# Kernel tuning notes

Measured on AMD Instinct MI355X. Metric: run time of the kernel, lower is better.

The kernel has to match this reference:

```python
import jax, jax.numpy as jnp
import numpy as np

OVERLAP_THRESHOLD = 0.5
NEG_POS_RATIO = 3
ALPHA = 1.0


def cxcy_to_xy(cxcy):
    return jnp.concatenate([cxcy[..., :2] - cxcy[..., 2:] / 2,
                            cxcy[..., :2] + cxcy[..., 2:] / 2], axis=-1)


def xy_to_cxcy(xy):
    return jnp.concatenate([(xy[..., :2] + xy[..., 2:]) / 2,
                            xy[..., 2:] - xy[..., :2]], axis=-1)


def cxcy_to_gcxgcy(cxcy, priors_cxcy):
    return jnp.concatenate([
        (cxcy[..., :2] - priors_cxcy[..., :2]) / (priors_cxcy[..., 2:] / 10.0),
        jnp.log(cxcy[..., 2:] / priors_cxcy[..., 2:]) * 5.0], axis=-1)


def jaccard(a, b):
    # a: [N,4] xy, b: [P,4] xy -> [N,P]
    lo = jnp.maximum(a[:, None, :2], b[None, :, :2])
    hi = jnp.minimum(a[:, None, 2:], b[None, :, 2:])
    inter = jnp.prod(jnp.clip(hi - lo, 0.0), axis=-1)  # [N,P]
    area_a = jnp.prod(a[:, 2:] - a[:, :2], axis=-1)  # [N]
    area_b = jnp.prod(b[:, 2:] - b[:, :2], axis=-1)  # [P]
    return inter / (area_a[:, None] + area_b[None, :] - inter)


def _match_one(boxes_i, labels_i, priors_cxcy, priors_xy):
    n_objects = boxes_i.shape[0]
    overlap = jaccard(boxes_i, priors_xy)  # [N,P]
    overlap_for_each_prior = overlap.max(axis=0)  # [P]
    object_for_each_prior = overlap.argmax(axis=0)  # [P]
    prior_for_each_object = overlap.argmax(axis=1)  # [N]
    # force each object to own its best prior
    object_for_each_prior = object_for_each_prior.at[prior_for_each_object].set(
        jnp.arange(n_objects))
    overlap_for_each_prior = overlap_for_each_prior.at[prior_for_each_object].set(1.0)
    labels_for_each_prior = labels_i[object_for_each_prior]
    labels_for_each_prior = jnp.where(overlap_for_each_prior < OVERLAP_THRESHOLD,
                                      0, labels_for_each_prior)
    matched = boxes_i[object_for_each_prior]  # [P,4]
    true_locs = cxcy_to_gcxgcy(xy_to_cxcy(matched), priors_cxcy)  # [P,4]
    return true_locs, labels_for_each_prior


def reference(predicted_locs, predicted_scores, boxes, labels, priors_cxcy):
    B, P, C = predicted_scores.shape
    priors_xy = cxcy_to_xy(priors_cxcy)
    true_locs, true_classes = jax.vmap(
        _match_one, in_axes=(0, 0, None, None))(boxes, labels, priors_cxcy, priors_xy)
    # true_locs: [B,P,4], true_classes: [B,P]
    positive = true_classes != 0  # [B,P]
    n_pos = positive.sum(axis=1)  # [B]
    n_pos_total = n_pos.sum()

    # SmoothL1 (beta=1, mean over selected elements = n_pos_total*4)
    d = predicted_locs - true_locs
    ad = jnp.abs(d)
    sl1 = jnp.where(ad < 1.0, 0.5 * d * d, ad - 0.5)  # [B,P,4]
    loc_loss = (sl1 * positive[..., None]).sum() / (n_pos_total.astype(jnp.float32) * 4.0)

    # per-prior cross-entropy
    logp = jax.nn.log_softmax(predicted_scores, axis=-1)  # [B,P,C]
    conf_all = -jnp.take_along_axis(logp, true_classes[..., None], axis=-1)[..., 0]  # [B,P]

    conf_pos_sum = jnp.where(positive, conf_all, 0.0).sum()
    conf_neg = jnp.where(positive, 0.0, conf_all)
    conf_neg_sorted = jnp.sort(conf_neg, axis=1)[:, ::-1]  # descending
    n_hard_neg = NEG_POS_RATIO * n_pos  # [B]
    rank = jnp.arange(P)[None, :]
    hard_neg_mask = rank < n_hard_neg[:, None]
    conf_hard_neg_sum = jnp.where(hard_neg_mask, conf_neg_sorted, 0.0).sum()

    conf_loss = (conf_hard_neg_sum + conf_pos_sum) / n_pos_total.astype(jnp.float32)
    return conf_loss + ALPHA * loc_loss


def setup_inputs() -> dict:
    key = jax.random.key(0)
    ks = jax.random.split(key, 7)
    B, P, C, N = 128, 8732, 21, 16
    predicted_locs = jax.random.normal(ks[0], (B, P, 4), dtype=jnp.float32)
    predicted_scores = jax.random.normal(ks[1], (B, P, C), dtype=jnp.float32)
    # valid xy boxes in [0,1]
    p1 = jax.random.uniform(ks[2], (B, N, 2)) * 0.85
    wh = jax.random.uniform(ks[3], (B, N, 2), minval=0.02, maxval=0.15)
    boxes = jnp.concatenate([p1, jnp.minimum(p1 + wh, 1.0)], axis=-1)
    labels = jax.random.randint(ks[4], (B, N), 1, C)
    cxcy = jax.random.uniform(ks[5], (P, 2))
    pwh = jax.random.uniform(ks[6], (P, 2), minval=0.05, maxval=0.5)
    priors_cxcy = jnp.concatenate([cxcy, pwh], axis=-1)
    return {"predicted_locs": predicted_locs, "predicted_scores": predicted_scores,
            "boxes": boxes, "labels": labels, "priors_cxcy": priors_cxcy}
```

## Files before the change

kernel.cpp:

```cpp
#include <hip/hip_runtime.h>


#define MAXN 16
#define MAXE 16

__device__ __forceinline__ float sl1f(float d) {
    float ad = fabsf(d);
    return ad < 1.0f ? 0.5f * d * d : ad - 0.5f;
}

__global__ __launch_bounds__(256) void k_pre(
    const float* __restrict__ boxes,
    const float* __restrict__ priors,
    int P, int N,
    int* __restrict__ pfo,
    int* __restrict__ npos,
    float* __restrict__ acc)
{
    __shared__ float rin[4], run[4];
    __shared__ int   rid[4];
    const int id = blockIdx.x;
    const int tid = threadIdx.x;
    const int lane = tid & 63, wid = tid >> 6;

    if (tid == 0 && (id % N) == 0) npos[id / N] = 0;
    if (id == 0 && tid < 2) ((unsigned*)acc)[tid] = 0u;

    const float* bp = boxes + (size_t)id * 4;
    const float bx1 = bp[0], by1 = bp[1], bx2 = bp[2], by2 = bp[3];
    const float ba = (bx2 - bx1) * (by2 - by1);

    float bi = -1.0f, bu = 1.0f; int idx = 0x7fffffff;
#pragma unroll 2
    for (int p = tid; p < P; p += 256) {
        float4 pr = ((const float4*)priors)[p];
        float px1 = pr.x - pr.z * 0.5f, py1 = pr.y - pr.w * 0.5f;
        float px2 = pr.x + pr.z * 0.5f, py2 = pr.y + pr.w * 0.5f;
        float parea = (px2 - px1) * (py2 - py1);
        float iw = fmaxf(fminf(bx2, px2) - fmaxf(bx1, px1), 0.0f);
        float ih = fmaxf(fminf(by2, py2) - fmaxf(by1, py1), 0.0f);
        float in = iw * ih;
        float un = ba + parea - in;
        if (in * bu > bi * un) { bi = in; bu = un; idx = p; }
    }
#pragma unroll
    for (int off = 32; off > 0; off >>= 1) {
        float oin = __shfl_down(bi, off);
        float oun = __shfl_down(bu, off);
        int   oid = __shfl_down(idx, off);
        float a = oin * bu, c = bi * oun;
        if (a > c || (a == c && oid < idx)) { bi = oin; bu = oun; idx = oid; }
    }
    if (lane == 0) { rin[wid] = bi; run[wid] = bu; rid[wid] = idx; }
    __syncthreads();
    if (tid == 0) {
        for (int w = 1; w < 4; w++) {
            float oin = rin[w], oun = run[w]; int oid = rid[w];
            float a = oin * bu, c = bi * oun;
            if (a > c || (a == c && oid < idx)) { bi = oin; bu = oun; idx = oid; }
        }
        pfo[id] = idx;
    }
}

template<int CT>
__global__ __launch_bounds__(256) void k_fused(
    const float* __restrict__ plocs,
    const float* __restrict__ scores,
    const float* __restrict__ boxes,
    const int*   __restrict__ labels,
    const float* __restrict__ priors,
    const int*   __restrict__ pfo,
    int P, int Crt, int N, int nchunk,
    float* __restrict__ conf_out,
    int*   __restrict__ npos,
    float* __restrict__ locpart,
    float* __restrict__ pospart)
{
    const int C = CT > 0 ? CT : Crt;
    extern __shared__ float sh[];
    __shared__ float sx1[MAXN], sy1[MAXN], sx2[MAXN], sy2[MAXN], barea[MAXN];
    __shared__ int   blab[MAXN], spfo[MAXN];
    __shared__ float redf[4], redp[4];
    __shared__ int   redi[4];

    const int b = blockIdx.y;
    const int tid = threadIdx.x;
    const int lane = tid & 63, wid = tid >> 6;
    if (N > MAXN) N = MAXN;
    const int p0 = blockIdx.x * 256;
    const int rows = min(256, P - p0);

    if (tid < N) {
        const float* bp = boxes + ((size_t)b * N + tid) * 4;
        float x1 = bp[0], y1 = bp[1], x2 = bp[2], y2 = bp[3];
        sx1[tid] = x1; sy1[tid] = y1; sx2[tid] = x2; sy2[tid] = y2;
        barea[tid] = (x2 - x1) * (y2 - y1);
        blab[tid] = labels[(size_t)b * N + tid];
        spfo[tid] = pfo[b * N + tid];
    }

    {
        const size_t f4base = ((size_t)b * P + p0) * C / 4;
        const int f4cnt = (rows * C + 3) / 4;
        const float4* __restrict__ s4 = (const float4*)scores;
        for (int j = tid; j < f4cnt; j += 256)
            ((float4*)sh)[j] = s4[f4base + j];
    }
    __syncthreads();

    const int p = p0 + tid;
    float locs = 0.0f, posc = 0.0f, conf = 0.0f;
    int np = 0;
    if (p < P) {
        float4 pr = ((const float4*)priors)[p];
        float px1 = pr.x - pr.z * 0.5f, py1 = pr.y - pr.w * 0.5f;
        float px2 = pr.x + pr.z * 0.5f, py2 = pr.y + pr.w * 0.5f;
        float parea = (px2 - px1) * (py2 - py1);
        float bi = -1.0f, bu = 1.0f; int bestn = 0;
#pragma unroll
        for (int n = 0; n < MAXN; n++) {
            if (n < N) {
                float iw = fmaxf(fminf(sx2[n], px2) - fmaxf(sx1[n], px1), 0.0f);
                float ih = fmaxf(fminf(sy2[n], py2) - fmaxf(sy1[n], py1), 0.0f);
                float in = iw * ih;
                float un = barea[n] + parea - in;
                if (in * bu > bi * un) { bi = in; bu = un; bestn = n; }
            }
        }
#pragma unroll
        for (int n = 0; n < MAXN; n++) {
            if (n < N && spfo[n] == p) { bestn = n; bi = 1.0f; bu = 1.0f; }
        }
        const int lab = (bi < 0.5f * bu) ? 0 : blab[bestn];

        const float* r = sh + tid * C;
        float m = -3.402823466e38f;
#pragma unroll
        for (int c = 0; c < C; c++) m = fmaxf(m, r[c]);
        float sum = 0.0f;
#pragma unroll
        for (int c = 0; c < C; c++) sum += __expf(r[c] - m);
        float ce = m + __logf(sum) - r[lab];

        if (lab != 0) {
            posc = ce; np = 1;
            int n = bestn;
            float cx = (sx1[n] + sx2[n]) * 0.5f, cy = (sy1[n] + sy2[n]) * 0.5f;
            float w = sx2[n] - sx1[n], h = sy2[n] - sy1[n];
            float g0 = (cx - pr.x) / (pr.z / 10.0f);
            float g1 = (cy - pr.y) / (pr.w / 10.0f);
            float g2 = logf(w / pr.z) * 5.0f;
            float g3 = logf(h / pr.w) * 5.0f;
            float4 pl = ((const float4*)plocs)[(size_t)b * P + p];
            locs = sl1f(pl.x - g0) + sl1f(pl.y - g1) + sl1f(pl.z - g2) + sl1f(pl.w - g3);
        } else {
            conf = ce;
        }
        conf_out[(size_t)b * P + p] = conf;
    }
#pragma unroll
    for (int off = 32; off > 0; off >>= 1) {
        locs += __shfl_down(locs, off);
        posc += __shfl_down(posc, off);
        np   += __shfl_down(np, off);
    }
    if (lane == 0) { redf[wid] = locs; redp[wid] = posc; redi[wid] = np; }
    __syncthreads();
    if (tid == 0) {
        float L = redf[0] + redf[1] + redf[2] + redf[3];
        float Pp = redp[0] + redp[1] + redp[2] + redp[3];
        int   c = redi[0] + redi[1] + redi[2] + redi[3];
        if (c) atomicAdd(&npos[b], c);
        locpart[b * nchunk + blockIdx.x] = L;
        pospart[b * nchunk + blockIdx.x] = Pp;
    }
}

__global__ __launch_bounds__(1024, 4) void k_hard(
    const float* __restrict__ conf,
    const int* __restrict__ npos,
    const float* __restrict__ locpart,
    const float* __restrict__ pospart,
    int P, int B, int nloc,
    float* __restrict__ acc,
    float* __restrict__ out)
{
    __shared__ int   redi[16 * 3];
    __shared__ float redf2[16];
    __shared__ int   redi2[16];
    __shared__ float rl[16], rp[16];
    __shared__ int   rn[16], is_last;
    const int b = blockIdx.x, tid = threadIdx.x;
    const int lane = tid & 63, wid = tid >> 6;
    const int nthr = blockDim.x, nw = nthr >> 6;
    const int ne = (P + nthr - 1) / nthr;
    long long kk = (long long)npos[b] * 3;
    int k = kk > P ? P : (int)kk;

    float S = 0.0f;
    if (k > 0) {
        unsigned e[MAXE];
#pragma unroll
        for (int j = 0; j < MAXE; j++) {
            int p = j * nthr + tid;
            e[j] = (j < ne && p < P) ? __float_as_uint(conf[(size_t)b * P + p]) : 0u;
        }

        unsigned lo = 0u, hi = 0x7F800000u;
        while (lo < hi) {
            unsigned span = hi - lo;
            if (span >= 8) {
                unsigned q = span >> 2;
                unsigned m1 = lo + q, m2 = lo + 2 * q, m3 = lo + 3 * q;
                int c1 = 0, c2 = 0, c3 = 0;
#pragma unroll
                for (int j = 0; j < MAXE; j++) {
                    if (j < ne) {
                        unsigned v = e[j];
                        c1 += (int)__popcll(__ballot(v >= m1));
                        c2 += (int)__popcll(__ballot(v >= m2));
                        c3 += (int)__popcll(__ballot(v >= m3));
                    }
                }
                if (lane == 0) {
                    redi[wid * 3 + 0] = c1; redi[wid * 3 + 1] = c2; redi[wid * 3 + 2] = c3;
                }
                __syncthreads();
                int C1 = 0, C2 = 0, C3 = 0;
                for (int w = 0; w < nw; w++) {
                    C1 += redi[w * 3 + 0]; C2 += redi[w * 3 + 1]; C3 += redi[w * 3 + 2];
                }
                __syncthreads();
                if      (C3 >= k) lo = m3;
                else if (C2 >= k) { lo = m2; hi = m3 - 1; }
                else if (C1 >= k) { lo = m1; hi = m2 - 1; }
                else              hi = m1 - 1;
            } else {
                unsigned mid = lo + ((span + 1) >> 1);
                int c = 0;
#pragma unroll
                for (int j = 0; j < MAXE; j++)
                    if (j < ne) c += (int)__popcll(__ballot(e[j] >= mid));
                if (lane == 0) redi[wid * 3] = c;
                __syncthreads();
                int Cc = 0;
                for (int w = 0; w < nw; w++) Cc += redi[w * 3];
                __syncthreads();
                if (Cc >= k) lo = mid; else hi = mid - 1;
            }
        }

        float t = __uint_as_float(lo);
        float sgt = 0.0f; int cgt = 0;
#pragma unroll
        for (int j = 0; j < MAXE; j++) {
            if (j < ne) {
                float v = __uint_as_float(e[j]);
                if (v > t) { sgt += v; cgt++; }
            }
        }
#pragma unroll
        for (int off = 32; off > 0; off >>= 1) {
            sgt += __shfl_down(sgt, off);
            cgt += __shfl_down(cgt, off);
        }
        if (lane == 0) { redf2[wid] = sgt; redi2[wid] = cgt; }
        __syncthreads();
        if (tid == 0) {
            int Cg = 0;
            for (int w = 0; w < nw; w++) { S += redf2[w]; Cg += redi2[w]; }
            S += (float)(k - Cg) * t;
        }
        __syncthreads();
    }

    if (tid == 0) {
        atomicAdd(&acc[0], S);
        __threadfence();
        unsigned tk = atomicAdd((unsigned*)(acc + 1), 1u);
        is_last = (tk == (unsigned)gridDim.x - 1) ? 1 : 0;
    }
    __syncthreads();
    if (is_last) {
        float lp = 0.0f, pp = 0.0f; int np = 0;
        for (int i = tid; i < nloc; i += nthr) { lp += locpart[i]; pp += pospart[i]; }
        for (int i = tid; i < B; i += nthr) np += npos[i];
#pragma unroll
        for (int off = 32; off > 0; off >>= 1) {
            lp += __shfl_down(lp, off);
            pp += __shfl_down(pp, off);
            np += __shfl_down(np, off);
        }
        if (lane == 0) { rl[wid] = lp; rp[wid] = pp; rn[wid] = np; }
        __syncthreads();
        if (tid == 0) {
            float L = 0.0f, Pp = 0.0f; int Np = 0;
            for (int w = 0; w < nw; w++) { L += rl[w]; Pp += rp[w]; Np += rn[w]; }
            float hard = atomicAdd(&acc[0], 0.0f);
            float npf = (float)Np;
            out[0] = (hard + Pp) / npf + L / (npf * 4.0f);
        }
    }
}

extern "C" void kernel_launch(void* const* d_in, const int* in_sizes, int n_in,
                              void* d_out, int out_size, void* d_ws, size_t ws_size,
                              hipStream_t stream)
{
    const float* plocs  = (const float*)d_in[0];
    const float* scores = (const float*)d_in[1];
    const float* boxes  = (const float*)d_in[2];
    const int*   labels = (const int*)d_in[3];
    const float* priors = (const float*)d_in[4];

    int P = in_sizes[4] / 4;
    int B = in_sizes[0] / (P * 4);
    int C = in_sizes[1] / (in_sizes[0] / 4);
    int N = in_sizes[3] / B;
    int nchunk = (P + 255) / 256;
    int nloc = B * nchunk;
    int BN = B * N;

    char* w = (char*)d_ws;
    float* slot    = (float*)w;  w += (size_t)B * P * sizeof(float);
    int*   npos    = (int*)w;    w += (size_t)B * sizeof(int);
    int*   pfo     = (int*)w;    w += (size_t)BN * sizeof(int);
    float* locpart = (float*)w;  w += (size_t)nloc * sizeof(float);
    float* pospart = (float*)w;  w += (size_t)nloc * sizeof(float);
    w = (char*)(((uintptr_t)w + 63) & ~(uintptr_t)63);
    float* acc     = (float*)w;

    k_pre<<<BN, 256, 0, stream>>>(boxes, priors, P, N, pfo, npos, acc);

    dim3 ga(nchunk, B);
    size_t smf = (size_t)256 * C * sizeof(float);
    if (C == 21) {
        k_fused<21><<<ga, 256, smf, stream>>>(plocs, scores, boxes, labels, priors,
                                              pfo, P, C, N, nchunk, slot, npos,
                                              locpart, pospart);
    } else {
        k_fused<0><<<ga, 256, smf, stream>>>(plocs, scores, boxes, labels, priors,
                                             pfo, P, C, N, nchunk, slot, npos,
                                             locpart, pospart);
    }

    k_hard<<<B, 1024, 0, stream>>>(slot, npos, locpart, pospart,
                                   P, B, nloc, acc, (float*)d_out);
}
```

Measured before the change: 213.8 us.

## Remove prior-matching pre-kernel and apply forced-match corrections inside hard-negative kernel

Drops the separate k_pre launch that found each object's best prior. The fused kernel now computes unforced matches and writes per-chunk positive counts instead of doing atomics. The hard-negative kernel recomputes each object's best prior per image and applies delta corrections to the loc, positive-CE and positive-count sums, then zeroes those priors' conf entries before selection. This saves one launch and its serial dependency, at the cost of extra per-block prior scanning in k_hard with 16 register accumulators per thread.

Measured after the change: 692.2 us. 224% more time.

```diff
diff --git a/kernel.cpp b/kernel.cpp
--- a/kernel.cpp
+++ b/kernel.cpp
@@ -7,60 +7,6 @@
 __device__ __forceinline__ float sl1f(float d) {
     float ad = fabsf(d);
     return ad < 1.0f ? 0.5f * d * d : ad - 0.5f;
-}
-
-__global__ __launch_bounds__(256) void k_pre(
-    const float* __restrict__ boxes,
-    const float* __restrict__ priors,
-    int P, int N,
-    int* __restrict__ pfo,
-    int* __restrict__ npos,
-    float* __restrict__ acc)
-{
-    __shared__ float rin[4], run[4];
-    __shared__ int   rid[4];
-    const int id = blockIdx.x;
-    const int tid = threadIdx.x;
-    const int lane = tid & 63, wid = tid >> 6;
-
-    if (tid == 0 && (id % N) == 0) npos[id / N] = 0;
-    if (id == 0 && tid < 2) ((unsigned*)acc)[tid] = 0u;
-
-    const float* bp = boxes + (size_t)id * 4;
-    const float bx1 = bp[0], by1 = bp[1], bx2 = bp[2], by2 = bp[3];
-    const float ba = (bx2 - bx1) * (by2 - by1);
-
-    float bi = -1.0f, bu = 1.0f; int idx = 0x7fffffff;
-#pragma unroll 2
-    for (int p = tid; p < P; p += 256) {
-        float4 pr = ((const float4*)priors)[p];
-        float px1 = pr.x - pr.z * 0.5f, py1 = pr.y - pr.w * 0.5f;
-        float px2 = pr.x + pr.z * 0.5f, py2 = pr.y + pr.w * 0.5f;
-        float parea = (px2 - px1) * (py2 - py1);
-        float iw = fmaxf(fminf(bx2, px2) - fmaxf(bx1, px1), 0.0f);
-        float ih = fmaxf(fminf(by2, py2) - fmaxf(by1, py1), 0.0f);
-        float in = iw * ih;
-        float un = ba + parea - in;
-        if (in * bu > bi * un) { bi = in; bu = un; idx = p; }
-    }
-#pragma unroll
-    for (int off = 32; off > 0; off >>= 1) {
-        float oin = __shfl_down(bi, off);
-        float oun = __shfl_down(bu, off);
-        int   oid = __shfl_down(idx, off);
-        float a = oin * bu, c = bi * oun;
-        if (a > c || (a == c && oid < idx)) { bi = oin; bu = oun; idx = oid; }
-    }
-    if (lane == 0) { rin[wid] = bi; run[wid] = bu; rid[wid] = idx; }
-    __syncthreads();
-    if (tid == 0) {
-        for (int w = 1; w < 4; w++) {
-            float oin = rin[w], oun = run[w]; int oid = rid[w];
-            float a = oin * bu, c = bi * oun;
-            if (a > c || (a == c && oid < idx)) { bi = oin; bu = oun; idx = oid; }
-        }
-        pfo[id] = idx;
-    }
 }
 
 template<int CT>
@@ -70,34 +16,35 @@
     const float* __restrict__ boxes,
     const int*   __restrict__ labels,
     const float* __restrict__ priors,
-    const int*   __restrict__ pfo,
     int P, int Crt, int N, int nchunk,
     float* __restrict__ conf_out,
-    int*   __restrict__ npos,
     float* __restrict__ locpart,
-    float* __restrict__ pospart)
+    float* __restrict__ pospart,
+    int*   __restrict__ nppart,
+    unsigned* __restrict__ acc)
 {
     const int C = CT > 0 ? CT : Crt;
     extern __shared__ float sh[];
-    __shared__ float sx1[MAXN], sy1[MAXN], sx2[MAXN], sy2[MAXN], barea[MAXN];
-    __shared__ int   blab[MAXN], spfo[MAXN];
+    __shared__ float sx1[MAXN], sy1[MAXN], sx2[MAXN], sy2[MAXN], sba[MAXN];
+    __shared__ int   blab[MAXN];
     __shared__ float redf[4], redp[4];
     __shared__ int   redi[4];
 
     const int b = blockIdx.y;
     const int tid = threadIdx.x;
     const int lane = tid & 63, wid = tid >> 6;
-    if (N > MAXN) N = MAXN;
+    int Nc = N > MAXN ? MAXN : N;
     const int p0 = blockIdx.x * 256;
     const int rows = min(256, P - p0);
 
-    if (tid < N) {
+    if (blockIdx.x == 0 && b == 0 && tid < 2) acc[tid] = 0u;
+
+    if (tid < Nc) {
         const float* bp = boxes + ((size_t)b * N + tid) * 4;
         float x1 = bp[0], y1 = bp[1], x2 = bp[2], y2 = bp[3];
         sx1[tid] = x1; sy1[tid] = y1; sx2[tid] = x2; sy2[tid] = y2;
-        barea[tid] = (x2 - x1) * (y2 - y1);
+        sba[tid] = (x2 - x1) * (y2 - y1);
         blab[tid] = labels[(size_t)b * N + tid];
-        spfo[tid] = pfo[b * N + tid];
     }
 
     {
@@ -120,28 +67,36 @@
         float bi = -1.0f, bu = 1.0f; int bestn = 0;
 #pragma unroll
         for (int n = 0; n < MAXN; n++) {
-            if (n < N) {
+            if (n < Nc) {
                 float iw = fmaxf(fminf(sx2[n], px2) - fmaxf(sx1[n], px1), 0.0f);
                 float ih = fmaxf(fminf(sy2[n], py2) - fmaxf(sy1[n], py1), 0.0f);
                 float in = iw * ih;
-                float un = barea[n] + parea - in;
+                float un = sba[n] + parea - in;
                 if (in * bu > bi * un) { bi = in; bu = un; bestn = n; }
             }
         }
-#pragma unroll
-        for (int n = 0; n < MAXN; n++) {
-            if (n < N && spfo[n] == p) { bestn = n; bi = 1.0f; bu = 1.0f; }
-        }
         const int lab = (bi < 0.5f * bu) ? 0 : blab[bestn];
 
         const float* r = sh + tid * C;
-        float m = -3.402823466e38f;
-#pragma unroll
-        for (int c = 0; c < C; c++) m = fmaxf(m, r[c]);
-        float sum = 0.0f;
-#pragma unroll
-        for (int c = 0; c < C; c++) sum += __expf(r[c] - m);
-        float ce = m + __logf(sum) - r[lab];
+        float ce;
+        if constexpr (CT > 0) {
+            float rv[CT];
+#pragma unroll
+            for (int c = 0; c < CT; c++) rv[c] = r[c];
+            float m = -3.402823466e38f;
+#pragma unroll
+            for (int c = 0; c < CT; c++) m = fmaxf(m, rv[c]);
+            float sum = 0.0f;
+#pragma unroll
+            for (int c = 0; c < CT; c++) sum += __expf(rv[c] - m);
+            ce = m + __logf(sum) - r[lab];
+        } else {
+            float m = -3.402823466e38f;
+            for (int c = 0; c < C; c++) m = fmaxf(m, r[c]);
+            float sum = 0.0f;
+            for (int c = 0; c < C; c++) sum += __expf(r[c] - m);
+            ce = m + __logf(sum) - r[lab];
+        }
 
         if (lab != 0) {
             posc = ce; np = 1;
@@ -168,37 +123,184 @@
     if (lane == 0) { redf[wid] = locs; redp[wid] = posc; redi[wid] = np; }
     __syncthreads();
     if (tid == 0) {
-        float L = redf[0] + redf[1] + redf[2] + redf[3];
-        float Pp = redp[0] + redp[1] + redp[2] + redp[3];
-        int   c = redi[0] + redi[1] + redi[2] + redi[3];
-        if (c) atomicAdd(&npos[b], c);
-        locpart[b * nchunk + blockIdx.x] = L;
-        pospart[b * nchunk + blockIdx.x] = Pp;
+        locpart[b * nchunk + blockIdx.x] = redf[0] + redf[1] + redf[2] + redf[3];
+        pospart[b * nchunk + blockIdx.x] = redp[0] + redp[1] + redp[2] + redp[3];
+        nppart [b * nchunk + blockIdx.x] = redi[0] + redi[1] + redi[2] + redi[3];
     }
 }
 
 __global__ __launch_bounds__(1024, 4) void k_hard(
+    const float* __restrict__ plocs,
+    const float* __restrict__ scores,
+    const float* __restrict__ boxes,
+    const int*   __restrict__ labels,
+    const float* __restrict__ priors,
     const float* __restrict__ conf,
-    const int* __restrict__ npos,
     const float* __restrict__ locpart,
     const float* __restrict__ pospart,
-    int P, int B, int nloc,
-    float* __restrict__ acc,
+    const int*   __restrict__ nppart,
+    int P, int C, int N, int nchunk, int B, int nloc,
+    float* __restrict__ hardpart,
+    float* __restrict__ locfix,
+    float* __restrict__ posfix,
+    int*   __restrict__ nposc,
+    unsigned* __restrict__ acc,
     float* __restrict__ out)
 {
-    __shared__ int   redi[16 * 3];
-    __shared__ float redf2[16];
-    __shared__ int   redi2[16];
-    __shared__ float rl[16], rp[16];
-    __shared__ int   rn[16], is_last;
+    __shared__ float sx1[MAXN], sy1[MAXN], sx2[MAXN], sy2[MAXN], sba[MAXN];
+    __shared__ int   blab[MAXN];
+    __shared__ float win[16 * MAXN], wun[16 * MAXN];
+    __shared__ int   widx[16 * MAXN];
+    __shared__ int   fixp[MAXN];
+    __shared__ float rfa[16], rfb[16];
+    __shared__ int   ria[16], rib[16];
+    __shared__ int   srch[16 * 3];
+    __shared__ int   s_np, is_last;
+    __shared__ float s_dloc, s_dpos;
+
     const int b = blockIdx.x, tid = threadIdx.x;
     const int lane = tid & 63, wid = tid >> 6;
     const int nthr = blockDim.x, nw = nthr >> 6;
+    int Nc = N > MAXN ? MAXN : N;
+
+    if (tid < Nc) {
+        const float* bp = boxes + ((size_t)b * N + tid) * 4;
+        float x1 = bp[0], y1 = bp[1], x2 = bp[2], y2 = bp[3];
+        sx1[tid] = x1; sy1[tid] = y1; sx2[tid] = x2; sy2[tid] = y2;
+        sba[tid] = (x2 - x1) * (y2 - y1);
+        blab[tid] = labels[(size_t)b * N + tid];
+    }
+    __syncthreads();
+
+    {
+        float bin[MAXN], bun[MAXN]; int bix[MAXN];
+#pragma unroll
+        for (int n = 0; n < MAXN; n++) { bin[n] = -1.0f; bun[n] = 1.0f; bix[n] = 0x7fffffff; }
+        for (int p = tid; p < P; p += nthr) {
+            float4 pr = ((const float4*)priors)[p];
+            float px1 = pr.x - pr.z * 0.5f, py1 = pr.y - pr.w * 0.5f;
+            float px2 = pr.x + pr.z * 0.5f, py2 = pr.y + pr.w * 0.5f;
+            float parea = (px2 - px1) * (py2 - py1);
+#pragma unroll
+            for (int n = 0; n < MAXN; n++) {
+                if (n < Nc) {
+                    float iw = fmaxf(fminf(sx2[n], px2) - fmaxf(sx1[n], px1), 0.0f);
+                    float ih = fmaxf(fminf(sy2[n], py2) - fmaxf(sy1[n], py1), 0.0f);
+                    float in = iw * ih;
+                    float un = sba[n] + parea - in;
+                    if (in * bun[n] > bin[n] * un) { bin[n] = in; bun[n] = un; bix[n] = p; }
+                }
+            }
+        }
+#pragma unroll
+        for (int n = 0; n < MAXN; n++) {
+            if (n < Nc) {
+                float i_ = bin[n], u_ = bun[n]; int x_ = bix[n];
+#pragma unroll
+                for (int off = 32; off > 0; off >>= 1) {
+                    float oi = __shfl_down(i_, off);
+                    float ou = __shfl_down(u_, off);
+                    int   ox = __shfl_down(x_, off);
+                    float a = oi * u_, c = i_ * ou;
+                    if (a > c || (a == c && ox < x_)) { i_ = oi; u_ = ou; x_ = ox; }
+                }
+                if (lane == 0) { win[wid * MAXN + n] = i_; wun[wid * MAXN + n] = u_; widx[wid * MAXN + n] = x_; }
+            }
+        }
+        __syncthreads();
+        if (tid < Nc) {
+            float i_ = win[tid], u_ = wun[tid]; int x_ = widx[tid];
+            for (int w = 1; w < nw; w++) {
+                float oi = win[w * MAXN + tid], ou = wun[w * MAXN + tid];
+                int   ox = widx[w * MAXN + tid];
+                float a = oi * u_, c = i_ * ou;
+                if (a > c || (a == c && ox < x_)) { i_ = oi; u_ = ou; x_ = ox; }
+            }
+            fixp[tid] = x_;
+        }
+        __syncthreads();
+    }
+
+    float dloc = 0.0f, dpos = 0.0f; int dnp = 0;
+    if (tid < Nc) {
+        int pn = fixp[tid];
+        bool active = true;
+        for (int n2 = tid + 1; n2 < Nc; n2++) if (fixp[n2] == pn) active = false;
+        if (active) {
+            float4 pr = ((const float4*)priors)[pn];
+            float px1 = pr.x - pr.z * 0.5f, py1 = pr.y - pr.w * 0.5f;
+            float px2 = pr.x + pr.z * 0.5f, py2 = pr.y + pr.w * 0.5f;
+            float parea = (px2 - px1) * (py2 - py1);
+            float bi = -1.0f, bu = 1.0f; int bestn = 0;
+#pragma unroll
+            for (int n = 0; n < MAXN; n++) {
+                if (n < Nc) {
+                    float iw = fmaxf(fminf(sx2[n], px2) - fmaxf(sx1[n], px1), 0.0f);
+                    float ih = fmaxf(fminf(sy2[n], py2) - fmaxf(sy1[n], py1), 0.0f);
+                    float in = iw * ih;
+                    float un = sba[n] + parea - in;
+                    if (in * bu > bi * un) { bi = in; bu = un; bestn = n; }
+                }
+            }
+            const int lab0 = (bi < 0.5f * bu) ? 0 : blab[bestn];
+
+            const float* r = scores + ((size_t)b * P + pn) * C;
+            float m = -3.402823466e38f;
+            for (int c = 0; c < C; c++) m = fmaxf(m, r[c]);
+            float sum = 0.0f;
+            for (int c = 0; c < C; c++) sum += __expf(r[c] - m);
+            const float lse = m + __logf(sum);
+
+            float4 pl = ((const float4*)plocs)[(size_t)b * P + pn];
+            {
+                int n = tid;
+                float cx = (sx1[n] + sx2[n]) * 0.5f, cy = (sy1[n] + sy2[n]) * 0.5f;
+                float w = sx2[n] - sx1[n], h = sy2[n] - sy1[n];
+                float g0 = (cx - pr.x) / (pr.z / 10.0f);
+                float g1 = (cy - pr.y) / (pr.w / 10.0f);
+                float g2 = logf(w / pr.z) * 5.0f;
+                float g3 = logf(h / pr.w) * 5.0f;
+                dloc = sl1f(pl.x - g0) + sl1f(pl.y - g1) + sl1f(pl.z - g2) + sl1f(pl.w - g3);
+                dpos = lse - r[blab[n]];
+            }
+            if (lab0 != 0) {
+                int n = bestn;
+                float cx = (sx1[n] + sx2[n]) * 0.5f, cy = (sy1[n] + sy2[n]) * 0.5f;
+                float w = sx2[n] - sx1[n], h = sy2[n] - sy1[n];
+                float g0 = (cx - pr.x) / (pr.z / 10.0f);
+                float g1 = (cy - pr.y) / (pr.w / 10.0f);
+                float g2 = logf(w / pr.z) * 5.0f;
+                float g3 = logf(h / pr.w) * 5.0f;
+                dloc -= sl1f(pl.x - g0) + sl1f(pl.y - g1) + sl1f(pl.z - g2) + sl1f(pl.w - g3);
+                dpos -= lse - r[lab0];
+            } else {
+                dnp = 1;
+            }
+        }
+    }
+    int npp = 0;
+    for (int i = tid; i < nchunk; i += nthr) npp += nppart[b * nchunk + i];
+#pragma unroll
+    for (int off = 32; off > 0; off >>= 1) {
+        dloc += __shfl_down(dloc, off);
+        dpos += __shfl_down(dpos, off);
+        dnp  += __shfl_down(dnp, off);
+        npp  += __shfl_down(npp, off);
+    }
+    if (lane == 0) { rfa[wid] = dloc; rfb[wid] = dpos; ria[wid] = dnp; rib[wid] = npp; }
+    __syncthreads();
+    if (tid == 0) {
+        float L = 0.0f, Pp = 0.0f; int a = 0, c = 0;
+        for (int w = 0; w < nw; w++) { L += rfa[w]; Pp += rfb[w]; a += ria[w]; c += rib[w]; }
+        s_dloc = L; s_dpos = Pp; s_np = c + a;
+    }
+    __syncthreads();
+    const int npos_b = s_np;
+    long long kk = (long long)npos_b * 3;
+    int k = kk > P ? P : (int)kk;
+
+    float S = 0.0f;
     const int ne = (P + nthr - 1) / nthr;
-    long long kk = (long long)npos[b] * 3;
-    int k = kk > P ? P : (int)kk;
-
-    float S = 0.0f;
     if (k > 0) {
         unsigned e[MAXE];
 #pragma unroll
@@ -206,7 +308,13 @@
             int p = j * nthr + tid;
             e[j] = (j < ne && p < P) ? __float_as_uint(conf[(size_t)b * P + p]) : 0u;
         }
-
+#pragma unroll
+        for (int j = 0; j < MAXE; j++) {
+            if (j < ne) {
+                int p = j * nthr + tid;
+                for (int n = 0; n < Nc; n++) if (fixp[n] == p) e[j] = 0u;
+            }
+        }
         unsigned lo = 0u, hi = 0x7F800000u;
         while (lo < hi) {
             unsigned span = hi - lo;
@@ -223,13 +331,11 @@
                         c3 += (int)__popcll(__ballot(v >= m3));
                     }
                 }
-                if (lane == 0) {
-                    redi[wid * 3 + 0] = c1; redi[wid * 3 + 1] = c2; redi[wid * 3 + 2] = c3;
-                }
+                if (lane == 0) { srch[wid * 3] = c1; srch[wid * 3 + 1] = c2; srch[wid * 3 + 2] = c3; }
                 __syncthreads();
                 int C1 = 0, C2 = 0, C3 = 0;
                 for (int w = 0; w < nw; w++) {
-                    C1 += redi[w * 3 + 0]; C2 += redi[w * 3 + 1]; C3 += redi[w * 3 + 2];
+                    C1 += srch[w * 3]; C2 += srch[w * 3 + 1]; C3 += srch[w * 3 + 2];
                 }
                 __syncthreads();
                 if      (C3 >= k) lo = m3;
@@ -242,15 +348,14 @@
 #pragma unroll
                 for (int j = 0; j < MAXE; j++)
                     if (j < ne) c += (int)__popcll(__ballot(e[j] >= mid));
-                if (lane == 0) redi[wid * 3] = c;
+                if (lane == 0) srch[wid * 3] = c;
                 __syncthreads();
                 int Cc = 0;
-                for (int w = 0; w < nw; w++) Cc += redi[w * 3];
+                for (int w = 0; w < nw; w++) Cc += srch[w * 3];
                 __syncthreads();
                 if (Cc >= k) lo = mid; else hi = mid - 1;
             }
         }
-
         float t = __uint_as_float(lo);
         float sgt = 0.0f; int cgt = 0;
 #pragma unroll
@@ -265,41 +370,47 @@
             sgt += __shfl_down(sgt, off);
             cgt += __shfl_down(cgt, off);
         }
-        if (lane == 0) { redf2[wid] = sgt; redi2[wid] = cgt; }
+        if (lane == 0) { rfa[wid] = sgt; ria[wid] = cgt; }
         __syncthreads();
         if (tid == 0) {
             int Cg = 0;
-            for (int w = 0; w < nw; w++) { S += redf2[w]; Cg += redi2[w]; }
+            for (int w = 0; w < nw; w++) { S += rfa[w]; Cg += ria[w]; }
             S += (float)(k - Cg) * t;
         }
         __syncthreads();
     }
 
     if (tid == 0) {
-        atomicAdd(&acc[0], S);
+        hardpart[b] = S;
+        locfix[b] = s_dloc;
+        posfix[b] = s_dpos;
+        nposc[b] = npos_b;
         __threadfence();
-        unsigned tk = atomicAdd((unsigned*)(acc + 1), 1u);
+        unsigned tk = atomicAdd(acc + 1, 1u);
         is_last = (tk == (unsigned)gridDim.x - 1) ? 1 : 0;
     }
     __syncthreads();
     if (is_last) {
-        float lp = 0.0f, pp = 0.0f; int np = 0;
+        __threadfence();
+        float lp = 0.0f, pp = 0.0f, hp = 0.0f; int np = 0;
         for (int i = tid; i < nloc; i += nthr) { lp += locpart[i]; pp += pospart[i]; }
-        for (int i = tid; i < B; i += nthr) np += npos[i];
+        for (int i = tid; i < B; i += nthr) {
+            lp += locfix[i]; pp += posfix[i]; hp += hardpart[i]; np += nposc[i];
+        }
 #pragma unroll
         for (int off = 32; off > 0; off >>= 1) {
             lp += __shfl_down(lp, off);
             pp += __shfl_down(pp, off);
+            hp += __shfl_down(hp, off);
             np += __shfl_down(np, off);
         }
-        if (lane == 0) { rl[wid] = lp; rp[wid] = pp; rn[wid] = np; }
+        if (lane == 0) { rfa[wid] = lp; rfb[wid] = pp; win[wid] = hp; ria[wid] = np; }
         __syncthreads();
         if (tid == 0) {
-            float L = 0.0f, Pp = 0.0f; int Np = 0;
-            for (int w = 0; w < nw; w++) { L += rl[w]; Pp += rp[w]; Np += rn[w]; }
-            float hard = atomicAdd(&acc[0], 0.0f);
+            float L = 0.0f, Pp = 0.0f, H = 0.0f; int Np = 0;
+            for (int w = 0; w < nw; w++) { L += rfa[w]; Pp += rfb[w]; H += win[w]; Np += ria[w]; }
             float npf = (float)Np;
-            out[0] = (hard + Pp) / npf + L / (npf * 4.0f);
+            out[0] = (H + Pp) / npf + L / (npf * 4.0f);
         }
     }
 }
@@ -320,31 +431,34 @@
     int N = in_sizes[3] / B;
     int nchunk = (P + 255) / 256;
     int nloc = B * nchunk;
-    int BN = B * N;
 
     char* w = (char*)d_ws;
-    float* slot    = (float*)w;  w += (size_t)B * P * sizeof(float);
-    int*   npos    = (int*)w;    w += (size_t)B * sizeof(int);
-    int*   pfo     = (int*)w;    w += (size_t)BN * sizeof(int);
-    float* locpart = (float*)w;  w += (size_t)nloc * sizeof(float);
-    float* pospart = (float*)w;  w += (size_t)nloc * sizeof(float);
+    float* conf     = (float*)w;  w += (size_t)B * P * sizeof(float);
+    float* locpart  = (float*)w;  w += (size_t)nloc * sizeof(float);
+    float* pospart  = (float*)w;  w += (size_t)nloc * sizeof(float);
+    int*   nppart   = (int*)w;    w += (size_t)nloc * sizeof(int);
+    float* hardpart = (float*)w;  w += (size_t)B * sizeof(float);
+    float* locfix   = (float*)w;  w += (size_t)B * sizeof(float);
+    float* posfix   = (float*)w;  w += (size_t)B * sizeof(float);
+    int*   nposc    = (int*)w;    w += (size_t)B * sizeof(int);
     w = (char*)(((uintptr_t)w + 63) & ~(uintptr_t)63);
-    float* acc     = (float*)w;
-
-    k_pre<<<BN, 256, 0, stream>>>(boxes, priors, P, N, pfo, npos, acc);
+    unsigned* acc   = (unsigned*)w;
 
     dim3 ga(nchunk, B);
     size_t smf = (size_t)256 * C * sizeof(float);
     if (C == 21) {
         k_fused<21><<<ga, 256, smf, stream>>>(plocs, scores, boxes, labels, priors,
-                                              pfo, P, C, N, nchunk, slot, npos,
-                                              locpart, pospart);
+                                              P, C, N, nchunk, conf,
+                                              locpart, pospart, nppart, acc);
     } else {
         k_fused<0><<<ga, 256, smf, stream>>>(plocs, scores, boxes, labels, priors,
-                                             pfo, P, C, N, nchunk, slot, npos,
-                                             locpart, pospart);
-    }
-
-    k_hard<<<B, 1024, 0, stream>>>(slot, npos, locpart, pospart,
-                                   P, B, nloc, acc, (float*)d_out);
+                                             P, C, N, nchunk, conf,
+                                             locpart, pospart, nppart, acc);
+    }
+
+    k_hard<<<B, 1024, 0, stream>>>(plocs, scores, boxes, labels, priors,
+                                   conf, locpart, pospart, nppart,
+                                   P, C, N, nchunk, B, nloc,
+                                   hardpart, locfix, posfix, nposc,
+                                   acc, (float*)d_out);
 }
```
